# Kernel tuning notes

Measured on AMD Instinct MI355X. Metric: run time of the kernel, lower is better.

The kernel has to match this reference:

```python
import jax, jax.numpy as jnp
import numpy as np

B, P, F, H, C, D = 512, 32, 16, 4, 32, 128   # graphs, nodes/graph, node feat, heads, head_dim, hidden
N = B * P
E_DIM = 5

def _lin(k, o, i):
    return jax.random.normal(k, (o, i)) * (1.0 / np.sqrt(i))

def setup_inputs():
    key = jax.random.key(0)
    ks = jax.random.split(key, 32)
    # fully-connected directed edges (no self loops) within each graph
    a = np.repeat(np.arange(P), P); b = np.tile(np.arange(P), P)
    m = a != b; a, b = a[m], b[m]
    off = (np.arange(B) * P)[:, None]
    src = (a[None, :] + off).reshape(-1); dst = (b[None, :] + off).reshape(-1)
    edge_index = jnp.asarray(np.stack([src, dst]), dtype=jnp.int32)
    E = src.size
    x = jax.random.normal(ks[0], (N, F))
    edge_attr = jax.random.normal(ks[1], (E, E_DIM))
    z = jnp.zeros
    return dict(
        x=x, edge_index=edge_index, edge_attr=edge_attr,
        W1l=_lin(ks[2], D, F), b1l=z(D), W1r=_lin(ks[3], D, F), b1r=z(D),
        W1e=_lin(ks[4], D, E_DIM), att1=jax.random.normal(ks[5], (1, H, C)) * 0.1, bias1=z(D),
        W2l=_lin(ks[6], D, D), b2l=z(D), W2r=_lin(ks[7], D, D), b2r=z(D),
        W2e=_lin(ks[8], D, E_DIM), att2=jax.random.normal(ks[9], (1, H, C)) * 0.1, bias2=z(D),
        Wc1=_lin(ks[10], D, D), bc1=z(D), Wc2=_lin(ks[11], 1, D), bc2=z(1),
        Ws1=_lin(ks[12], D, D), bs1=z(D), Ws2=_lin(ks[13], 1, D), bs2=z(1),
        Wn1=_lin(ks[14], D, D), bn1=z(D), Wn2=_lin(ks[15], 1, D), bn2=z(1),
    )

def _gatv2(x, src, dst, edge_attr, Wl, bl, Wr, br, We, att, bias):
    # PyG GATv2Conv, concat=True, heads=H, out_channels=C, edge_dim=E_DIM, add_self_loops=False
    E = src.shape[0]
    xl = x @ Wl.T + bl                                   # [N, H*C] messages (source side)
    xr = x @ Wr.T + br                                   # [N, H*C] destination side
    e = (xl[src] + xr[dst] + edge_attr @ We.T).reshape(E, H, C)
    g = jax.nn.leaky_relu(e, 0.2)
    score = jnp.sum(g * att, axis=-1)                    # [E, H]
    smax = jax.ops.segment_max(score, dst, num_segments=N)
    ex = jnp.exp(score - smax[dst])
    denom = jax.ops.segment_sum(ex, dst, num_segments=N)
    alpha = ex / (denom[dst] + 1e-16)                    # segment softmax over in-edges of dst
    msg = xl[src].reshape(E, H, C) * alpha[..., None]
    return jax.ops.segment_sum(msg, dst, num_segments=N).reshape(N, H * C) + bias

def _mlp(h, W1, b1, W2, b2):
    return jax.nn.relu(h @ W1.T + b1) @ W2.T + b2

def reference(x, edge_index, edge_attr, W1l, b1l, W1r, b1r, W1e, att1, bias1,
              W2l, b2l, W2r, b2r, W2e, att2, bias2,
              Wc1, bc1, Wc2, bc2, Ws1, bs1, Ws2, bs2, Wn1, bn1, Wn2, bn2):
    src, dst = edge_index[0], edge_index[1]
    h = _gatv2(x, src, dst, edge_attr, W1l, b1l, W1r, b1r, W1e, att1, bias1)
    hb = h.reshape(B, P, D)
    h = (hb - hb.mean(axis=1, keepdims=True)).reshape(N, D)   # MeanSubtractionNorm per graph
    h = jax.nn.relu(h)
    h = jax.nn.relu(_gatv2(h, src, dst, edge_attr, W2l, b2l, W2r, b2r, W2e, att2, bias2))
    g = h.reshape(B, P, D).mean(axis=1)                       # global_mean_pool (equal-size graphs)
    value = _mlp(g, Wc1, bc1, Wc2, bc2)                       # critic        [B, 1]
    src_logits = _mlp(h, Ws1, bs1, Ws2, bs2).reshape(B, P)    # source_actor, dense per graph
    noop = _mlp(g, Wn1, bn1, Wn2, bn2)                        # noop_actor    [B, 1]
    return jnp.concatenate([value, noop, src_logits], axis=1) # [B, P+2]
```

## Files before the change

### kernel.cpp

```cpp
#include <hip/hip_runtime.h>

#define PP    32
#define FF    16
#define HH    4
#define CC    32
#define DD    128
#define EDIM  5
#define EPG   992
#define NB    512

template <int CTRL>
__device__ __forceinline__ float dpp_add(float v) {
    int t = __builtin_amdgcn_update_dpp(0, __builtin_bit_cast(int, v), CTRL, 0xF, 0xF, true);
    return v + __builtin_bit_cast(float, t);
}
template <int CTRL>
__device__ __forceinline__ float dpp_mov(float v) {
    int t = __builtin_amdgcn_update_dpp(0, __builtin_bit_cast(int, v), CTRL, 0xF, 0xF, true);
    return __builtin_bit_cast(float, t);
}
template <int DK>
__device__ __forceinline__ float qb(float v) {
    int t = __builtin_amdgcn_update_dpp(0, __builtin_bit_cast(int, v), DK * 0x55, 0xF, 0xF, true);
    return __builtin_bit_cast(float, t);
}
__device__ __forceinline__ float red64(float v) {
    v = dpp_add<0x111>(v);
    v = dpp_add<0x112>(v);
    v = dpp_add<0x114>(v);
    v = dpp_add<0x118>(v);
    v = dpp_add<0x142>(v);
    v = dpp_add<0x143>(v);
    return v;
}
__device__ __forceinline__ float redquad(float v) {
    v = dpp_add<0xB1>(v);
    v = dpp_add<0x4E>(v);
    return v;
}
__device__ __forceinline__ float maxquad(float v) {
    v = fmaxf(v, dpp_mov<0xB1>(v));
    v = fmaxf(v, dpp_mov<0x4E>(v));
    return v;
}

template <int DK>
__device__ __forceinline__ float score_step(const float* __restrict__ sDst, int d, int ch0,
                                            const float* we, const float* at, const float* xl,
                                            const float* eaC)
{
    const float e0 = qb<DK>(eaC[0]), e1 = qb<DK>(eaC[1]), e2 = qb<DK>(eaC[2]),
                e3 = qb<DK>(eaC[3]), e4 = qb<DK>(eaC[4]);
    float xr[8];
    *(float4*)(xr)     = *(const float4*)(sDst + d * DD + ch0);
    *(float4*)(xr + 4) = *(const float4*)(sDst + d * DD + ch0 + 4);
    float acc0 = 0.f, acc1 = 0.f;
#pragma unroll
    for (int c = 0; c < 8; ++c) {
        float v = xl[c] + xr[c];
        const float* w = we + c * EDIM;
        v = fmaf(w[0], e0, v); v = fmaf(w[1], e1, v); v = fmaf(w[2], e2, v);
        v = fmaf(w[3], e3, v); v = fmaf(w[4], e4, v);
        v = fmaf(0.4f, fabsf(v), 0.6f * v);
        if (c & 1) acc1 = fmaf(v, at[c], acc1);
        else       acc0 = fmaf(v, at[c], acc0);
    }
    return redquad(acc0 + acc1);
}

__device__ __forceinline__ void attention(const float* __restrict__ eattr,
                                          const float* __restrict__ We, const float* __restrict__ att,
                                          const float* __restrict__ bias,
                                          const float* __restrict__ sMsg, const float* __restrict__ sDst,
                                          float* __restrict__ sS, float* __restrict__ sOut,
                                          int tid, long eBase, bool relu)
{
    {
        const int s   = tid >> 4;
        const int h4  = (tid >> 2) & 3;
        const int c4  = tid & 3;
        const int ch0 = (tid & 15) * 8;
        float we[40], at[8], xl[8];
#pragma unroll
        for (int q = 0; q < 10; ++q)
            *(float4*)(we + q * 4) = *(const float4*)(We + ch0 * EDIM + q * 4);
        *(float4*)(at)     = *(const float4*)(att + ch0);
        *(float4*)(at + 4) = *(const float4*)(att + ch0 + 4);
        *(float4*)(xl)     = *(const float4*)(sMsg + s * DD + ch0);
        *(float4*)(xl + 4) = *(const float4*)(sMsg + s * DD + ch0 + 4);

        float eaC[5], eaN[5];
        {
            const int d = c4;
            int jj = d - (d > s);
            if (jj > 30) jj = 30;
            const float* ea = eattr + (eBase + s * 31 + jj) * EDIM;
#pragma unroll
            for (int q = 0; q < 5; ++q) eaC[q] = ea[q];
        }
        for (int d0 = 0; d0 < PP; d0 += 4) {
            {
                int d = d0 + 4 + c4;
                if (d > 31) d = 31;
                int jj = d - (d > s);
                if (jj > 30) jj = 30;
                const float* ea = eattr + (eBase + s * 31 + jj) * EDIM;
#pragma unroll
                for (int q = 0; q < 5; ++q) eaN[q] = ea[q];
            }
            const float r0 = score_step<0>(sDst, d0 + 0, ch0, we, at, xl, eaC);
            const float r1 = score_step<1>(sDst, d0 + 1, ch0, we, at, xl, eaC);
            const float r2 = score_step<2>(sDst, d0 + 2, ch0, we, at, xl, eaC);
            const float r3 = score_step<3>(sDst, d0 + 3, ch0, we, at, xl, eaC);
            const float rw = (c4 == 0) ? r0 : (c4 == 1) ? r1 : (c4 == 2) ? r2 : r3;
            sS[s * DD + (d0 + c4) * HH + h4] = rw;
#pragma unroll
            for (int q = 0; q < 5; ++q) eaC[q] = eaN[q];
        }
    }
    __syncthreads();
    {
        const int col = tid >> 2;
        const int r   = tid & 3;
        const int dd  = col >> 2;
        float v[8];
        float mx = -3.4e38f;
#pragma unroll
        for (int i = 0; i < 8; ++i) {
            const int s = r * 8 + i;
            v[i] = sS[s * DD + col];
            mx = (s == dd) ? mx : fmaxf(mx, v[i]);
        }
        mx = maxquad(mx);
        float sum = 0.f;
#pragma unroll
        for (int i = 0; i < 8; ++i) {
            const int s = r * 8 + i;
            float ex = __expf(v[i] - mx);
            ex = (s == dd) ? 0.f : ex;
            v[i] = ex; sum += ex;
        }
        sum = redquad(sum);
        const float inv = 1.f / (sum + 1e-16f);
#pragma unroll
        for (int i = 0; i < 8; ++i)
            sS[(r * 8 + i) * DD + col] = v[i] * inv;
    }
    __syncthreads();
    {
        const int d = tid >> 4, sub = tid & 15;
#pragma unroll
        for (int half = 0; half < 2; ++half) {
            const int ch4 = half * 16 + sub;
            const int idx = d * HH + (ch4 >> 3);
            const float* bp = bias + ch4 * 4;
            float4 acc = make_float4(bp[0], bp[1], bp[2], bp[3]);
#pragma unroll
            for (int s = 0; s < PP; ++s) {
                const float a = sS[s * DD + idx];
                const float4 xv = *(const float4*)(sMsg + s * DD + ch4 * 4);
                acc.x = fmaf(a, xv.x, acc.x);
                acc.y = fmaf(a, xv.y, acc.y);
                acc.z = fmaf(a, xv.z, acc.z);
                acc.w = fmaf(a, xv.w, acc.w);
            }
            if (relu) {
                acc.x = fmaxf(acc.x, 0.f); acc.y = fmaxf(acc.y, 0.f);
                acc.z = fmaxf(acc.z, 0.f); acc.w = fmaxf(acc.w, 0.f);
            }
            *(float4*)(sOut + d * DD + ch4 * 4) = acc;
        }
    }
}

extern "C" __global__ void __launch_bounds__(512, 4)
planetwars_gnn_kernel(const float* __restrict__ x, const float* __restrict__ eattr,
                      const float* __restrict__ W1l, const float* __restrict__ b1l,
                      const float* __restrict__ W1r, const float* __restrict__ b1r,
                      const float* __restrict__ W1e, const float* __restrict__ att1, const float* __restrict__ bias1,
                      const float* __restrict__ W2l, const float* __restrict__ b2l,
                      const float* __restrict__ W2r, const float* __restrict__ b2r,
                      const float* __restrict__ W2e, const float* __restrict__ att2, const float* __restrict__ bias2,
                      const float* __restrict__ Wc1, const float* __restrict__ bc1,
                      const float* __restrict__ Wc2, const float* __restrict__ bc2,
                      const float* __restrict__ Ws1, const float* __restrict__ bs1,
                      const float* __restrict__ Ws2, const float* __restrict__ bs2,
                      const float* __restrict__ Wn1, const float* __restrict__ bn1,
                      const float* __restrict__ Wn2, const float* __restrict__ bn2,
                      float* __restrict__ out)
{
    __shared__ __align__(16) float sA[PP * DD];
    __shared__ __align__(16) float sB[PP * DD];
    __shared__ __align__(16) float sH[PP * DD];
    __shared__ __align__(16) float sU[PP * DD];

    const int tid = threadIdx.x;
    const int g = blockIdx.x;
    const long eBase = (long)g * EPG;

    sU[tid] = x[g * PP * FF + tid];
    __syncthreads();

    {
        const int j = tid & 127, d0 = (tid >> 7) * 8;
        float wl[16], wr[16];
#pragma unroll
        for (int q = 0; q < 4; ++q) {
            *(float4*)(wl + q * 4) = *(const float4*)(W1l + j * FF + q * 4);
            *(float4*)(wr + q * 4) = *(const float4*)(W1r + j * FF + q * 4);
        }
        const float bl = b1l[j], br = b1r[j];
#pragma unroll
        for (int i = 0; i < 8; ++i) {
            const float* xr = sU + (d0 + i) * FF;
            float al = bl, ar = br;
#pragma unroll
            for (int k = 0; k < FF; ++k) {
                const float xv = xr[k];
                al = fmaf(wl[k], xv, al);
                ar = fmaf(wr[k], xv, ar);
            }
            sA[(d0 + i) * DD + j] = al;
            sB[(d0 + i) * DD + j] = ar;
        }
    }
    __syncthreads();

    attention(eattr, W1e, att1, bias1, sA, sB, sU, sH, tid, eBase, false);
    __syncthreads();

    {
        const int col = tid >> 2, r = tid & 3;
        float v[8];
        float ssum = 0.f;
#pragma unroll
        for (int i = 0; i < 8; ++i) {
            v[i] = sH[(r * 8 + i) * DD + col];
            ssum += v[i];
        }
        ssum = redquad(ssum);
        const float mn = ssum * (1.0f / 32.0f);
#pragma unroll
        for (int i = 0; i < 8; ++i)
            sH[(r * 8 + i) * DD + col] = fmaxf(v[i] - mn, 0.f);
    }
    __syncthreads();

    {
        const int jj = tid & 63, d0 = (tid >> 6) * 4;
        float accL0[4], accL1[4], accR0[4], accR1[4];
        const float bl0 = b2l[jj], bl1 = b2l[jj + 64];
        const float br0 = b2r[jj], br1 = b2r[jj + 64];
#pragma unroll
        for (int i = 0; i < 4; ++i) { accL0[i] = bl0; accL1[i] = bl1; accR0[i] = br0; accR1[i] = br1; }
        const float* WL0 = W2l + jj * DD;
        const float* WL1 = W2l + (jj + 64) * DD;
        const float* WR0 = W2r + jj * DD;
        const float* WR1 = W2r + (jj + 64) * DD;
        for (int k8 = 0; k8 < 16; ++k8) {
            const float4 l00 = *(const float4*)(WL0 + k8 * 8), l01 = *(const float4*)(WL0 + k8 * 8 + 4);
            const float4 l10 = *(const float4*)(WL1 + k8 * 8), l11 = *(const float4*)(WL1 + k8 * 8 + 4);
            const float4 r00 = *(const float4*)(WR0 + k8 * 8), r01 = *(const float4*)(WR0 + k8 * 8 + 4);
            const float4 r10 = *(const float4*)(WR1 + k8 * 8), r11 = *(const float4*)(WR1 + k8 * 8 + 4);
#pragma unroll
            for (int i = 0; i < 4; ++i) {
                const float4 a0 = *(const float4*)(sH + (d0 + i) * DD + k8 * 8);
                const float4 a1 = *(const float4*)(sH + (d0 + i) * DD + k8 * 8 + 4);
                accL0[i] = fmaf(l00.x, a0.x, accL0[i]); accL0[i] = fmaf(l00.y, a0.y, accL0[i]);
                accL0[i] = fmaf(l00.z, a0.z, accL0[i]); accL0[i] = fmaf(l00.w, a0.w, accL0[i]);
                accL0[i] = fmaf(l01.x, a1.x, accL0[i]); accL0[i] = fmaf(l01.y, a1.y, accL0[i]);
                accL0[i] = fmaf(l01.z, a1.z, accL0[i]); accL0[i] = fmaf(l01.w, a1.w, accL0[i]);
                accL1[i] = fmaf(l10.x, a0.x, accL1[i]); accL1[i] = fmaf(l10.y, a0.y, accL1[i]);
                accL1[i] = fmaf(l10.z, a0.z, accL1[i]); accL1[i] = fmaf(l10.w, a0.w, accL1[i]);
                accL1[i] = fmaf(l11.x, a1.x, accL1[i]); accL1[i] = fmaf(l11.y, a1.y, accL1[i]);
                accL1[i] = fmaf(l11.w, a1.w, accL1[i]); accL1[i] = fmaf(l11.z, a1.z, accL1[i]);
                accR0[i] = fmaf(r00.x, a0.x, accR0[i]); accR0[i] = fmaf(r00.y, a0.y, accR0[i]);
                accR0[i] = fmaf(r00.z, a0.z, accR0[i]); accR0[i] = fmaf(r00.w, a0.w, accR0[i]);
                accR0[i] = fmaf(r01.x, a1.x, accR0[i]); accR0[i] = fmaf(r01.y, a1.y, accR0[i]);
                accR0[i] = fmaf(r01.z, a1.z, accR0[i]); accR0[i] = fmaf(r01.w, a1.w, accR0[i]);
                accR1[i] = fmaf(r10.x, a0.x, accR1[i]); accR1[i] = fmaf(r10.y, a0.y, accR1[i]);
                accR1[i] = fmaf(r10.z, a0.z, accR1[i]); accR1[i] = fmaf(r10.w, a0.w, accR1[i]);
                accR1[i] = fmaf(r11.x, a1.x, accR1[i]); accR1[i] = fmaf(r11.y, a1.y, accR1[i]);
                accR1[i] = fmaf(r11.z, a1.z, accR1[i]); accR1[i] = fmaf(r11.w, a1.w, accR1[i]);
            }
        }
#pragma unroll
        for (int i = 0; i < 4; ++i) {
            sA[(d0 + i) * DD + jj]      = accL0[i];
            sA[(d0 + i) * DD + jj + 64] = accL1[i];
            sB[(d0 + i) * DD + jj]      = accR0[i];
            sB[(d0 + i) * DD + jj + 64] = accR1[i];
        }
    }
    __syncthreads();

    attention(eattr, W2e, att2, bias2, sA, sB, sU, sH, tid, eBase, true);
    __syncthreads();

    {
        const int col = tid >> 2, r = tid & 3;
        float ssum = 0.f;
#pragma unroll
        for (int i = 0; i < 8; ++i) ssum += sH[(r * 8 + i) * DD + col];
        ssum = redquad(ssum);
        if (r == 0) sU[col] = ssum * (1.0f / 32.0f);
    }
    __syncthreads();

    {
        const int jj = tid & 63, d0 = (tid >> 6) * 4;
        const float b0 = bs1[jj], b1 = bs1[jj + 64];
        float acc0[4], acc1[4];
#pragma unroll
        for (int i = 0; i < 4; ++i) { acc0[i] = b0; acc1[i] = b1; }
        const float* W0 = Ws1 + jj * DD;
        const float* W1 = Ws1 + (jj + 64) * DD;
        for (int k8 = 0; k8 < 16; ++k8) {
            const float4 w00 = *(const float4*)(W0 + k8 * 8), w01 = *(const float4*)(W0 + k8 * 8 + 4);
            const float4 w10 = *(const float4*)(W1 + k8 * 8), w11 = *(const float4*)(W1 + k8 * 8 + 4);
#pragma unroll
            for (int i = 0; i < 4; ++i) {
                const float4 a0 = *(const float4*)(sH + (d0 + i) * DD + k8 * 8);
                const float4 a1 = *(const float4*)(sH + (d0 + i) * DD + k8 * 8 + 4);
                acc0[i] = fmaf(w00.x, a0.x, acc0[i]); acc0[i] = fmaf(w00.y, a0.y, acc0[i]);
                acc0[i] = fmaf(w00.z, a0.z, acc0[i]); acc0[i] = fmaf(w00.w, a0.w, acc0[i]);
                acc0[i] = fmaf(w01.x, a1.x, acc0[i]); acc0[i] = fmaf(w01.y, a1.y, acc0[i]);
                acc0[i] = fmaf(w01.z, a1.z, acc0[i]); acc0[i] = fmaf(w01.w, a1.w, acc0[i]);
                acc1[i] = fmaf(w10.x, a0.x, acc1[i]); acc1[i] = fmaf(w10.y, a0.y, acc1[i]);
                acc1[i] = fmaf(w10.z, a0.z, acc1[i]); acc1[i] = fmaf(w10.w, a0.w, acc1[i]);
                acc1[i] = fmaf(w11.x, a1.x, acc1[i]); acc1[i] = fmaf(w11.y, a1.y, acc1[i]);
                acc1[i] = fmaf(w11.z, a1.z, acc1[i]); acc1[i] = fmaf(w11.w, a1.w, acc1[i]);
            }
        }
        const float ws2a = Ws2[jj], ws2b = Ws2[jj + 64];
        const float bias2s = bs2[0];
#pragma unroll
        for (int i = 0; i < 4; ++i) {
            const float t = fmaf(fmaxf(acc0[i], 0.f), ws2a, fmaxf(acc1[i], 0.f) * ws2b);
            const float r = red64(t);
            if ((tid & 63) == 63) out[g * 34 + 2 + d0 + i] = r + bias2s;
        }
    }

    if (tid < 128) {
        const int w = tid >> 6, j = tid & 63;
        const float* Wa = (w ? Wn1 : Wc1);
        const float* ba = (w ? bn1 : bc1);
        const float* Wb = (w ? Wn2 : Wc2);
        const float  bb = (w ? bn2 : bc2)[0];
        float h0 = ba[j], h1 = ba[j + 64];
        const float* R0 = Wa + j * DD;
        const float* R1 = Wa + (j + 64) * DD;
#pragma unroll
        for (int k8 = 0; k8 < 16; ++k8) {
            const float4 g0 = *(const float4*)(sU + k8 * 8);
            const float4 g1 = *(const float4*)(sU + k8 * 8 + 4);
            const float4 p00 = *(const float4*)(R0 + k8 * 8), p01 = *(const float4*)(R0 + k8 * 8 + 4);
            const float4 p10 = *(const float4*)(R1 + k8 * 8), p11 = *(const float4*)(R1 + k8 * 8 + 4);
            h0 = fmaf(p00.x, g0.x, h0); h0 = fmaf(p00.y, g0.y, h0);
            h0 = fmaf(p00.z, g0.z, h0); h0 = fmaf(p00.w, g0.w, h0);
            h0 = fmaf(p01.x, g1.x, h0); h0 = fmaf(p01.y, g1.y, h0);
            h0 = fmaf(p01.z, g1.z, h0); h0 = fmaf(p01.w, g1.w, h0);
            h1 = fmaf(p10.x, g0.x, h1); h1 = fmaf(p10.y, g0.y, h1);
            h1 = fmaf(p10.z, g0.z, h1); h1 = fmaf(p10.w, g0.w, h1);
            h1 = fmaf(p11.x, g1.x, h1); h1 = fmaf(p11.y, g1.y, h1);
            h1 = fmaf(p11.z, g1.z, h1); h1 = fmaf(p11.w, g1.w, h1);
        }
        const float t = fmaf(fmaxf(h0, 0.f), Wb[j], fmaxf(h1, 0.f) * Wb[j + 64]);
        const float r = red64(t);
        if (j == 63) out[g * 34 + w] = r + bb;
    }
}

extern "C" void kernel_launch(void* const* d_in, const int* in_sizes, int n_in,
                              void* d_out, int out_size, void* d_ws, size_t ws_size,
                              hipStream_t stream)
{
    (void)in_sizes; (void)n_in; (void)d_ws; (void)ws_size; (void)out_size;
    planetwars_gnn_kernel<<<dim3(NB), dim3(512), 0, stream>>>(
        (const float*)d_in[0], (const float*)d_in[2],
        (const float*)d_in[3], (const float*)d_in[4], (const float*)d_in[5], (const float*)d_in[6],
        (const float*)d_in[7], (const float*)d_in[8], (const float*)d_in[9],
        (const float*)d_in[10], (const float*)d_in[11], (const float*)d_in[12], (const float*)d_in[13],
        (const float*)d_in[14], (const float*)d_in[15], (const float*)d_in[16],
        (const float*)d_in[17], (const float*)d_in[18], (const float*)d_in[19], (const float*)d_in[20],
        (const float*)d_in[21], (const float*)d_in[22], (const float*)d_in[23], (const float*)d_in[24],
        (const float*)d_in[25], (const float*)d_in[26], (const float*)d_in[27], (const float*)d_in[28],
        (float*)d_out);
}
```

Before: 254.0 us.

## Double block size to 1024 threads and halve per-thread work in GAT stages

Launches 1024 threads per graph instead of 512 and gives each thread half as much work in the node projections, the edge scoring and the aggregation. Each thread now handles 4 channels per head, and the per-head score is reduced with a quad DPP add plus a ds_swizzle xor-4 add. This replaces the old scheme of 8 channels per thread with DPP broadcasts of prefetched edge attributes. Softmax and the head MLPs stay on the first 512 threads, and the critic/noop MLP moves to threads 512-639 so it runs alongside the source actor. The aim is more parallelism and fewer registers per thread, at the cost of dropping edge-attribute prefetching and of redundant edge-attribute loads. The launch bound of 1024 threads with 8 minimum blocks may constrain registers heavily.

```diff
diff --git a/kernel.cpp b/kernel.cpp
--- a/kernel.cpp
+++ b/kernel.cpp
@@ -19,11 +19,6 @@
     int t = __builtin_amdgcn_update_dpp(0, __builtin_bit_cast(int, v), CTRL, 0xF, 0xF, true);
     return __builtin_bit_cast(float, t);
 }
-template <int DK>
-__device__ __forceinline__ float qb(float v) {
-    int t = __builtin_amdgcn_update_dpp(0, __builtin_bit_cast(int, v), DK * 0x55, 0xF, 0xF, true);
-    return __builtin_bit_cast(float, t);
-}
 __device__ __forceinline__ float red64(float v) {
     v = dpp_add<0x111>(v);
     v = dpp_add<0x112>(v);
@@ -43,29 +38,9 @@
     v = fmaxf(v, dpp_mov<0x4E>(v));
     return v;
 }
-
-template <int DK>
-__device__ __forceinline__ float score_step(const float* __restrict__ sDst, int d, int ch0,
-                                            const float* we, const float* at, const float* xl,
-                                            const float* eaC)
-{
-    const float e0 = qb<DK>(eaC[0]), e1 = qb<DK>(eaC[1]), e2 = qb<DK>(eaC[2]),
-                e3 = qb<DK>(eaC[3]), e4 = qb<DK>(eaC[4]);
-    float xr[8];
-    *(float4*)(xr)     = *(const float4*)(sDst + d * DD + ch0);
-    *(float4*)(xr + 4) = *(const float4*)(sDst + d * DD + ch0 + 4);
-    float acc0 = 0.f, acc1 = 0.f;
-#pragma unroll
-    for (int c = 0; c < 8; ++c) {
-        float v = xl[c] + xr[c];
-        const float* w = we + c * EDIM;
-        v = fmaf(w[0], e0, v); v = fmaf(w[1], e1, v); v = fmaf(w[2], e2, v);
-        v = fmaf(w[3], e3, v); v = fmaf(w[4], e4, v);
-        v = fmaf(0.4f, fabsf(v), 0.6f * v);
-        if (c & 1) acc1 = fmaf(v, at[c], acc1);
-        else       acc0 = fmaf(v, at[c], acc0);
-    }
-    return redquad(acc0 + acc1);
+__device__ __forceinline__ float swz_xor4_add(float v) {
+    int t = __builtin_amdgcn_ds_swizzle(__builtin_bit_cast(int, v), 0x101F);
+    return v + __builtin_bit_cast(float, t);
 }
 
 __device__ __forceinline__ void attention(const float* __restrict__ eattr,
@@ -76,50 +51,42 @@
                                           int tid, long eBase, bool relu)
 {
     {
-        const int s   = tid >> 4;
-        const int h4  = (tid >> 2) & 3;
-        const int c4  = tid & 3;
-        const int ch0 = (tid & 15) * 8;
-        float we[40], at[8], xl[8];
-#pragma unroll
-        for (int q = 0; q < 10; ++q)
+        const int s   = tid >> 5;
+        const int h4  = (tid >> 3) & 3;
+        const int ch0 = (tid & 31) * 4;
+        float we[20], at[4], xl[4];
+#pragma unroll
+        for (int q = 0; q < 5; ++q)
             *(float4*)(we + q * 4) = *(const float4*)(We + ch0 * EDIM + q * 4);
-        *(float4*)(at)     = *(const float4*)(att + ch0);
-        *(float4*)(at + 4) = *(const float4*)(att + ch0 + 4);
-        *(float4*)(xl)     = *(const float4*)(sMsg + s * DD + ch0);
-        *(float4*)(xl + 4) = *(const float4*)(sMsg + s * DD + ch0 + 4);
-
-        float eaC[5], eaN[5];
-        {
-            const int d = c4;
+        *(float4*)(at) = *(const float4*)(att + ch0);
+        *(float4*)(xl) = *(const float4*)(sMsg + s * DD + ch0);
+
+        for (int d = 0; d < PP; ++d) {
             int jj = d - (d > s);
             if (jj > 30) jj = 30;
             const float* ea = eattr + (eBase + s * 31 + jj) * EDIM;
-#pragma unroll
-            for (int q = 0; q < 5; ++q) eaC[q] = ea[q];
-        }
-        for (int d0 = 0; d0 < PP; d0 += 4) {
-            {
-                int d = d0 + 4 + c4;
-                if (d > 31) d = 31;
-                int jj = d - (d > s);
-                if (jj > 30) jj = 30;
-                const float* ea = eattr + (eBase + s * 31 + jj) * EDIM;
-#pragma unroll
-                for (int q = 0; q < 5; ++q) eaN[q] = ea[q];
+            const float e0 = ea[0], e1 = ea[1], e2 = ea[2], e3 = ea[3], e4 = ea[4];
+            float xr[4];
+            *(float4*)(xr) = *(const float4*)(sDst + d * DD + ch0);
+            float acc0 = 0.f, acc1 = 0.f;
+#pragma unroll
+            for (int c = 0; c < 4; ++c) {
+                float v = xl[c] + xr[c];
+                const float* w = we + c * EDIM;
+                v = fmaf(w[0], e0, v); v = fmaf(w[1], e1, v); v = fmaf(w[2], e2, v);
+                v = fmaf(w[3], e3, v); v = fmaf(w[4], e4, v);
+                v = fmaf(0.4f, fabsf(v), 0.6f * v);
+                if (c & 1) acc1 = fmaf(v, at[c], acc1);
+                else       acc0 = fmaf(v, at[c], acc0);
             }
-            const float r0 = score_step<0>(sDst, d0 + 0, ch0, we, at, xl, eaC);
-            const float r1 = score_step<1>(sDst, d0 + 1, ch0, we, at, xl, eaC);
-            const float r2 = score_step<2>(sDst, d0 + 2, ch0, we, at, xl, eaC);
-            const float r3 = score_step<3>(sDst, d0 + 3, ch0, we, at, xl, eaC);
-            const float rw = (c4 == 0) ? r0 : (c4 == 1) ? r1 : (c4 == 2) ? r2 : r3;
-            sS[s * DD + (d0 + c4) * HH + h4] = rw;
-#pragma unroll
-            for (int q = 0; q < 5; ++q) eaC[q] = eaN[q];
-        }
-    }
-    __syncthreads();
-    {
+            float r = redquad(acc0 + acc1);
+            r = swz_xor4_add(r);
+            if ((tid & 7) == (d & 7))
+                sS[s * DD + d * HH + h4] = r;
+        }
+    }
+    __syncthreads();
+    if (tid < 512) {
         const int col = tid >> 2;
         const int r   = tid & 3;
         const int dd  = col >> 2;
@@ -148,32 +115,27 @@
     }
     __syncthreads();
     {
-        const int d = tid >> 4, sub = tid & 15;
-#pragma unroll
-        for (int half = 0; half < 2; ++half) {
-            const int ch4 = half * 16 + sub;
-            const int idx = d * HH + (ch4 >> 3);
-            const float* bp = bias + ch4 * 4;
-            float4 acc = make_float4(bp[0], bp[1], bp[2], bp[3]);
-#pragma unroll
-            for (int s = 0; s < PP; ++s) {
-                const float a = sS[s * DD + idx];
-                const float4 xv = *(const float4*)(sMsg + s * DD + ch4 * 4);
-                acc.x = fmaf(a, xv.x, acc.x);
-                acc.y = fmaf(a, xv.y, acc.y);
-                acc.z = fmaf(a, xv.z, acc.z);
-                acc.w = fmaf(a, xv.w, acc.w);
-            }
-            if (relu) {
-                acc.x = fmaxf(acc.x, 0.f); acc.y = fmaxf(acc.y, 0.f);
-                acc.z = fmaxf(acc.z, 0.f); acc.w = fmaxf(acc.w, 0.f);
-            }
-            *(float4*)(sOut + d * DD + ch4 * 4) = acc;
-        }
-    }
-}
-
-extern "C" __global__ void __launch_bounds__(512, 4)
+        const int d = tid >> 5, ch4 = tid & 31;
+        const int idx = d * HH + (ch4 >> 3);
+        float4 acc = *(const float4*)(bias + ch4 * 4);
+#pragma unroll
+        for (int s = 0; s < PP; ++s) {
+            const float a = sS[s * DD + idx];
+            const float4 xv = *(const float4*)(sMsg + s * DD + ch4 * 4);
+            acc.x = fmaf(a, xv.x, acc.x);
+            acc.y = fmaf(a, xv.y, acc.y);
+            acc.z = fmaf(a, xv.z, acc.z);
+            acc.w = fmaf(a, xv.w, acc.w);
+        }
+        if (relu) {
+            acc.x = fmaxf(acc.x, 0.f); acc.y = fmaxf(acc.y, 0.f);
+            acc.z = fmaxf(acc.z, 0.f); acc.w = fmaxf(acc.w, 0.f);
+        }
+        *(float4*)(sOut + d * DD + ch4 * 4) = acc;
+    }
+}
+
+extern "C" __global__ void __launch_bounds__(1024, 8)
 planetwars_gnn_kernel(const float* __restrict__ x, const float* __restrict__ eattr,
                       const float* __restrict__ W1l, const float* __restrict__ b1l,
                       const float* __restrict__ W1r, const float* __restrict__ b1r,
@@ -198,11 +160,11 @@
     const int g = blockIdx.x;
     const long eBase = (long)g * EPG;
 
-    sU[tid] = x[g * PP * FF + tid];
+    if (tid < PP * FF) sU[tid] = x[g * PP * FF + tid];
     __syncthreads();
 
     {
-        const int j = tid & 127, d0 = (tid >> 7) * 8;
+        const int j = tid & 127, d0 = (tid >> 7) * 4;
         float wl[16], wr[16];
 #pragma unroll
         for (int q = 0; q < 4; ++q) {
@@ -211,7 +173,7 @@
         }
         const float bl = b1l[j], br = b1r[j];
 #pragma unroll
-        for (int i = 0; i < 8; ++i) {
+        for (int i = 0; i < 4; ++i) {
             const float* xr = sU + (d0 + i) * FF;
             float al = bl, ar = br;
 #pragma unroll
@@ -229,7 +191,7 @@
     attention(eattr, W1e, att1, bias1, sA, sB, sU, sH, tid, eBase, false);
     __syncthreads();
 
-    {
+    if (tid < 512) {
         const int col = tid >> 2, r = tid & 3;
         float v[8];
         float ssum = 0.f;
@@ -247,49 +209,34 @@
     __syncthreads();
 
     {
-        const int jj = tid & 63, d0 = (tid >> 6) * 4;
-        float accL0[4], accL1[4], accR0[4], accR1[4];
-        const float bl0 = b2l[jj], bl1 = b2l[jj + 64];
-        const float br0 = b2r[jj], br1 = b2r[jj + 64];
-#pragma unroll
-        for (int i = 0; i < 4; ++i) { accL0[i] = bl0; accL1[i] = bl1; accR0[i] = br0; accR1[i] = br1; }
-        const float* WL0 = W2l + jj * DD;
-        const float* WL1 = W2l + (jj + 64) * DD;
-        const float* WR0 = W2r + jj * DD;
-        const float* WR1 = W2r + (jj + 64) * DD;
+        const int jj = tid & 127, d0 = (tid >> 7) * 4;
+        float accL[4], accR[4];
+        const float bl = b2l[jj], br = b2r[jj];
+#pragma unroll
+        for (int i = 0; i < 4; ++i) { accL[i] = bl; accR[i] = br; }
+        const float* WL = W2l + jj * DD;
+        const float* WR = W2r + jj * DD;
         for (int k8 = 0; k8 < 16; ++k8) {
-            const float4 l00 = *(const float4*)(WL0 + k8 * 8), l01 = *(const float4*)(WL0 + k8 * 8 + 4);
-            const float4 l10 = *(const float4*)(WL1 + k8 * 8), l11 = *(const float4*)(WL1 + k8 * 8 + 4);
-            const float4 r00 = *(const float4*)(WR0 + k8 * 8), r01 = *(const float4*)(WR0 + k8 * 8 + 4);
-            const float4 r10 = *(const float4*)(WR1 + k8 * 8), r11 = *(const float4*)(WR1 + k8 * 8 + 4);
+            const float4 l0 = *(const float4*)(WL + k8 * 8), l1 = *(const float4*)(WL + k8 * 8 + 4);
+            const float4 r0 = *(const float4*)(WR + k8 * 8), r1 = *(const float4*)(WR + k8 * 8 + 4);
 #pragma unroll
             for (int i = 0; i < 4; ++i) {
                 const float4 a0 = *(const float4*)(sH + (d0 + i) * DD + k8 * 8);
                 const float4 a1 = *(const float4*)(sH + (d0 + i) * DD + k8 * 8 + 4);
-                accL0[i] = fmaf(l00.x, a0.x, accL0[i]); accL0[i] = fmaf(l00.y, a0.y, accL0[i]);
-                accL0[i] = fmaf(l00.z, a0.z, accL0[i]); accL0[i] = fmaf(l00.w, a0.w, accL0[i]);
-                accL0[i] = fmaf(l01.x, a1.x, accL0[i]); accL0[i] = fmaf(l01.y, a1.y, accL0[i]);
-                accL0[i] = fmaf(l01.z, a1.z, accL0[i]); accL0[i] = fmaf(l01.w, a1.w, accL0[i]);
-                accL1[i] = fmaf(l10.x, a0.x, accL1[i]); accL1[i] = fmaf(l10.y, a0.y, accL1[i]);
-                accL1[i] = fmaf(l10.z, a0.z, accL1[i]); accL1[i] = fmaf(l10.w, a0.w, accL1[i]);
-                accL1[i] = fmaf(l11.x, a1.x, accL1[i]); accL1[i] = fmaf(l11.y, a1.y, accL1[i]);
-                accL1[i] = fmaf(l11.w, a1.w, accL1[i]); accL1[i] = fmaf(l11.z, a1.z, accL1[i]);
-                accR0[i] = fmaf(r00.x, a0.x, accR0[i]); accR0[i] = fmaf(r00.y, a0.y, accR0[i]);
-                accR0[i] = fmaf(r00.z, a0.z, accR0[i]); accR0[i] = fmaf(r00.w, a0.w, accR0[i]);
-                accR0[i] = fmaf(r01.x, a1.x, accR0[i]); accR0[i] = fmaf(r01.y, a1.y, accR0[i]);
-                accR0[i] = fmaf(r01.z, a1.z, accR0[i]); accR0[i] = fmaf(r01.w, a1.w, accR0[i]);
-                accR1[i] = fmaf(r10.x, a0.x, accR1[i]); accR1[i] = fmaf(r10.y, a0.y, accR1[i]);
-                accR1[i] = fmaf(r10.z, a0.z, accR1[i]); accR1[i] = fmaf(r10.w, a0.w, accR1[i]);
-                accR1[i] = fmaf(r11.x, a1.x, accR1[i]); accR1[i] = fmaf(r11.y, a1.y, accR1[i]);
-                accR1[i] = fmaf(r11.z, a1.z, accR1[i]); accR1[i] = fmaf(r11.w, a1.w, accR1[i]);
+                accL[i] = fmaf(l0.x, a0.x, accL[i]); accL[i] = fmaf(l0.y, a0.y, accL[i]);
+                accL[i] = fmaf(l0.z, a0.z, accL[i]); accL[i] = fmaf(l0.w, a0.w, accL[i]);
+                accL[i] = fmaf(l1.x, a1.x, accL[i]); accL[i] = fmaf(l1.y, a1.y, accL[i]);
+                accL[i] = fmaf(l1.z, a1.z, accL[i]); accL[i] = fmaf(l1.w, a1.w, accL[i]);
+                accR[i] = fmaf(r0.x, a0.x, accR[i]); accR[i] = fmaf(r0.y, a0.y, accR[i]);
+                accR[i] = fmaf(r0.z, a0.z, accR[i]); accR[i] = fmaf(r0.w, a0.w, accR[i]);
+                accR[i] = fmaf(r1.x, a1.x, accR[i]); accR[i] = fmaf(r1.y, a1.y, accR[i]);
+                accR[i] = fmaf(r1.z, a1.z, accR[i]); accR[i] = fmaf(r1.w, a1.w, accR[i]);
             }
         }
 #pragma unroll
         for (int i = 0; i < 4; ++i) {
-            sA[(d0 + i) * DD + jj]      = accL0[i];
-            sA[(d0 + i) * DD + jj + 64] = accL1[i];
-            sB[(d0 + i) * DD + jj]      = accR0[i];
-            sB[(d0 + i) * DD + jj + 64] = accR1[i];
+            sA[(d0 + i) * DD + jj] = accL[i];
+            sB[(d0 + i) * DD + jj] = accR[i];
         }
     }
     __syncthreads();
@@ -297,7 +244,7 @@
     attention(eattr, W2e, att2, bias2, sA, sB, sU, sH, tid, eBase, true);
     __syncthreads();
 
-    {
+    if (tid < 512) {
         const int col = tid >> 2, r = tid & 3;
         float ssum = 0.f;
 #pragma unroll
@@ -307,7 +254,7 @@
     }
     __syncthreads();
 
-    {
+    if (tid < 512) {
         const int jj = tid & 63, d0 = (tid >> 6) * 4;
         const float b0 = bs1[jj], b1 = bs1[jj + 64];
         float acc0[4], acc1[4];
@@ -340,10 +287,9 @@
             const float r = red64(t);
             if ((tid & 63) == 63) out[g * 34 + 2 + d0 + i] = r + bias2s;
         }
-    }
-
-    if (tid < 128) {
-        const int w = tid >> 6, j = tid & 63;
+    } else if (tid < 640) {
+        const int t = tid - 512;
+        const int w = t >> 6, j = t & 63;
         const float* Wa = (w ? Wn1 : Wc1);
         const float* ba = (w ? bn1 : bc1);
         const float* Wb = (w ? Wn2 : Wc2);
@@ -364,10 +310,10 @@
             h1 = fmaf(p10.x, g0.x, h1); h1 = fmaf(p10.y, g0.y, h1);
             h1 = fmaf(p10.z, g0.z, h1); h1 = fmaf(p10.w, g0.w, h1);
             h1 = fmaf(p11.x, g1.x, h1); h1 = fmaf(p11.y, g1.y, h1);
-            h1 = fmaf(p11.z, g1.z, h1); h1 = fmaf(p11.w, g1.w, h1);
-        }
-        const float t = fmaf(fmaxf(h0, 0.f), Wb[j], fmaxf(h1, 0.f) * Wb[j + 64]);
-        const float r = red64(t);
+            h1 = fmaf(p11.w, g1.w, h1); h1 = fmaf(p11.z, g1.z, h1);
+        }
+        const float tt = fmaf(fmaxf(h0, 0.f), Wb[j], fmaxf(h1, 0.f) * Wb[j + 64]);
+        const float r = red64(tt);
         if (j == 63) out[g * 34 + w] = r + bb;
     }
 }
@@ -377,7 +323,7 @@
                               hipStream_t stream)
 {
     (void)in_sizes; (void)n_in; (void)d_ws; (void)ws_size; (void)out_size;
-    planetwars_gnn_kernel<<<dim3(NB), dim3(512), 0, stream>>>(
+    planetwars_gnn_kernel<<<dim3(NB), dim3(1024), 0, stream>>>(
         (const float*)d_in[0], (const float*)d_in[2],
         (const float*)d_in[3], (const float*)d_in[4], (const float*)d_in[5], (const float*)d_in[6],
         (const float*)d_in[7], (const float*)d_in[8], (const float*)d_in[9],
```

Measured after the change: 335.1 us. +31.9%, slower.

## Remap attention score threads to 4 channels each and loop source halves

Applied to the files above, without the earlier changes.

Reworks the GATv2 score computation so each thread covers 4 channels instead of 8 and handles two source-node halves in sequence. The reduction across a head's 32 channels now uses a quad DPP add plus a ds_swizzle xor-4 add. Edge attributes are loaded directly per destination, replacing the DPP quad-broadcast and prefetch pipelining. This aims to cut register pressure (we[20] instead of we[40]) and redundant work, at the cost of more redundant edge-attribute global loads and a swizzle step per score.

```diff
diff --git a/kernel.cpp b/kernel.cpp
--- a/kernel.cpp
+++ b/kernel.cpp
@@ -19,11 +19,6 @@
     int t = __builtin_amdgcn_update_dpp(0, __builtin_bit_cast(int, v), CTRL, 0xF, 0xF, true);
     return __builtin_bit_cast(float, t);
 }
-template <int DK>
-__device__ __forceinline__ float qb(float v) {
-    int t = __builtin_amdgcn_update_dpp(0, __builtin_bit_cast(int, v), DK * 0x55, 0xF, 0xF, true);
-    return __builtin_bit_cast(float, t);
-}
 __device__ __forceinline__ float red64(float v) {
     v = dpp_add<0x111>(v);
     v = dpp_add<0x112>(v);
@@ -43,29 +38,9 @@
     v = fmaxf(v, dpp_mov<0x4E>(v));
     return v;
 }
-
-template <int DK>
-__device__ __forceinline__ float score_step(const float* __restrict__ sDst, int d, int ch0,
-                                            const float* we, const float* at, const float* xl,
-                                            const float* eaC)
-{
-    const float e0 = qb<DK>(eaC[0]), e1 = qb<DK>(eaC[1]), e2 = qb<DK>(eaC[2]),
-                e3 = qb<DK>(eaC[3]), e4 = qb<DK>(eaC[4]);
-    float xr[8];
-    *(float4*)(xr)     = *(const float4*)(sDst + d * DD + ch0);
-    *(float4*)(xr + 4) = *(const float4*)(sDst + d * DD + ch0 + 4);
-    float acc0 = 0.f, acc1 = 0.f;
-#pragma unroll
-    for (int c = 0; c < 8; ++c) {
-        float v = xl[c] + xr[c];
-        const float* w = we + c * EDIM;
-        v = fmaf(w[0], e0, v); v = fmaf(w[1], e1, v); v = fmaf(w[2], e2, v);
-        v = fmaf(w[3], e3, v); v = fmaf(w[4], e4, v);
-        v = fmaf(0.4f, fabsf(v), 0.6f * v);
-        if (c & 1) acc1 = fmaf(v, at[c], acc1);
-        else       acc0 = fmaf(v, at[c], acc0);
-    }
-    return redquad(acc0 + acc1);
+__device__ __forceinline__ float swz_xor4_add(float v) {
+    int t = __builtin_amdgcn_ds_swizzle(__builtin_bit_cast(int, v), 0x101F);
+    return v + __builtin_bit_cast(float, t);
 }
 
 __device__ __forceinline__ void attention(const float* __restrict__ eattr,
@@ -76,46 +51,51 @@
                                           int tid, long eBase, bool relu)
 {
     {
-        const int s   = tid >> 4;
-        const int h4  = (tid >> 2) & 3;
-        const int c4  = tid & 3;
-        const int ch0 = (tid & 15) * 8;
-        float we[40], at[8], xl[8];
-#pragma unroll
-        for (int q = 0; q < 10; ++q)
+        const int h4  = (tid >> 3) & 3;
+        const int c8  = tid & 7;
+        const int ch0 = (tid & 31) * 4;
+        float we[20], at[4];
+#pragma unroll
+        for (int q = 0; q < 5; ++q)
             *(float4*)(we + q * 4) = *(const float4*)(We + ch0 * EDIM + q * 4);
-        *(float4*)(at)     = *(const float4*)(att + ch0);
-        *(float4*)(at + 4) = *(const float4*)(att + ch0 + 4);
-        *(float4*)(xl)     = *(const float4*)(sMsg + s * DD + ch0);
-        *(float4*)(xl + 4) = *(const float4*)(sMsg + s * DD + ch0 + 4);
-
-        float eaC[5], eaN[5];
-        {
-            const int d = c4;
-            int jj = d - (d > s);
-            if (jj > 30) jj = 30;
-            const float* ea = eattr + (eBase + s * 31 + jj) * EDIM;
-#pragma unroll
-            for (int q = 0; q < 5; ++q) eaC[q] = ea[q];
-        }
-        for (int d0 = 0; d0 < PP; d0 += 4) {
-            {
-                int d = d0 + 4 + c4;
-                if (d > 31) d = 31;
-                int jj = d - (d > s);
-                if (jj > 30) jj = 30;
-                const float* ea = eattr + (eBase + s * 31 + jj) * EDIM;
-#pragma unroll
-                for (int q = 0; q < 5; ++q) eaN[q] = ea[q];
-            }
-            const float r0 = score_step<0>(sDst, d0 + 0, ch0, we, at, xl, eaC);
-            const float r1 = score_step<1>(sDst, d0 + 1, ch0, we, at, xl, eaC);
-            const float r2 = score_step<2>(sDst, d0 + 2, ch0, we, at, xl, eaC);
-            const float r3 = score_step<3>(sDst, d0 + 3, ch0, we, at, xl, eaC);
-            const float rw = (c4 == 0) ? r0 : (c4 == 1) ? r1 : (c4 == 2) ? r2 : r3;
-            sS[s * DD + (d0 + c4) * HH + h4] = rw;
-#pragma unroll
-            for (int q = 0; q < 5; ++q) eaC[q] = eaN[q];
+        *(float4*)(at) = *(const float4*)(att + ch0);
+
+        for (int half = 0; half < 2; ++half) {
+            const int s = (tid >> 5) + half * 16;
+            float xl[4];
+            *(float4*)(xl) = *(const float4*)(sMsg + s * DD + ch0);
+            const float* eaRow = eattr + (eBase + (long)s * 31) * EDIM;
+            for (int d0 = 0; d0 < PP; d0 += 2) {
+                const int d1 = d0 + 1;
+                int j0 = d0 - (d0 > s); if (j0 > 30) j0 = 30;
+                int j1 = d1 - (d1 > s); if (j1 > 30) j1 = 30;
+                const float* ea0 = eaRow + j0 * EDIM;
+                const float* ea1 = eaRow + j1 * EDIM;
+                const float e00 = ea0[0], e01 = ea0[1], e02 = ea0[2], e03 = ea0[3], e04 = ea0[4];
+                const float e10 = ea1[0], e11 = ea1[1], e12 = ea1[2], e13 = ea1[3], e14 = ea1[4];
+                float xr0[4], xr1[4];
+                *(float4*)(xr0) = *(const float4*)(sDst + d0 * DD + ch0);
+                *(float4*)(xr1) = *(const float4*)(sDst + d1 * DD + ch0);
+                float a00 = 0.f, a01 = 0.f, a10 = 0.f, a11 = 0.f;
+#pragma unroll
+                for (int c = 0; c < 4; ++c) {
+                    const float* w = we + c * EDIM;
+                    float v0 = xl[c] + xr0[c];
+                    v0 = fmaf(w[0], e00, v0); v0 = fmaf(w[1], e01, v0); v0 = fmaf(w[2], e02, v0);
+                    v0 = fmaf(w[3], e03, v0); v0 = fmaf(w[4], e04, v0);
+                    v0 = fmaf(0.4f, fabsf(v0), 0.6f * v0);
+                    float v1 = xl[c] + xr1[c];
+                    v1 = fmaf(w[0], e10, v1); v1 = fmaf(w[1], e11, v1); v1 = fmaf(w[2], e12, v1);
+                    v1 = fmaf(w[3], e13, v1); v1 = fmaf(w[4], e14, v1);
+                    v1 = fmaf(0.4f, fabsf(v1), 0.6f * v1);
+                    if (c & 1) { a01 = fmaf(v0, at[c], a01); a11 = fmaf(v1, at[c], a11); }
+                    else       { a00 = fmaf(v0, at[c], a00); a10 = fmaf(v1, at[c], a10); }
+                }
+                const float r0 = swz_xor4_add(redquad(a00 + a01));
+                const float r1 = swz_xor4_add(redquad(a10 + a11));
+                if (c8 == (d0 & 7)) sS[s * DD + d0 * HH + h4] = r0;
+                if (c8 == (d1 & 7)) sS[s * DD + d1 * HH + h4] = r1;
+            }
         }
     }
     __syncthreads();
@@ -273,7 +253,7 @@
                 accL1[i] = fmaf(l10.x, a0.x, accL1[i]); accL1[i] = fmaf(l10.y, a0.y, accL1[i]);
                 accL1[i] = fmaf(l10.z, a0.z, accL1[i]); accL1[i] = fmaf(l10.w, a0.w, accL1[i]);
                 accL1[i] = fmaf(l11.x, a1.x, accL1[i]); accL1[i] = fmaf(l11.y, a1.y, accL1[i]);
-                accL1[i] = fmaf(l11.w, a1.w, accL1[i]); accL1[i] = fmaf(l11.z, a1.z, accL1[i]);
+                accL1[i] = fmaf(l11.z, a1.z, accL1[i]); accL1[i] = fmaf(l11.w, a1.w, accL1[i]);
                 accR0[i] = fmaf(r00.x, a0.x, accR0[i]); accR0[i] = fmaf(r00.y, a0.y, accR0[i]);
                 accR0[i] = fmaf(r00.z, a0.z, accR0[i]); accR0[i] = fmaf(r00.w, a0.w, accR0[i]);
                 accR0[i] = fmaf(r01.x, a1.x, accR0[i]); accR0[i] = fmaf(r01.y, a1.y, accR0[i]);
```

Result: slower. 310.8 us (+22.4%).
